# Kernel optimization log

Hardware: AMD Instinct MI355X
Metric: run time of the kernel (lower is better)

## Reference

```python
import jax, jax.numpy as jnp
import numpy as np

BN_EPS = 1e-5
B, N, C, H, HID = 16, 1024, 512, 8, 2048


def _bn(x, g, b, m, v):
    # inference-mode BatchNorm1d over channel dim (last axis here, since the
    # torch code transposes to (B,C,N) before BN and back after)
    return (x - m) * (g * jax.lax.rsqrt(v + BN_EPS)) + b


def _stage(x, w, bias, g, be, m, v):
    # Linear -> BN -> ReLU fused chain
    return jax.nn.relu(_bn(x @ w.T + bias, g, be, m, v))


def setup_inputs() -> dict:
    key = jax.random.key(0)
    ks = iter(jax.random.split(key, 64))
    d = {"x": jax.random.normal(next(ks), (B, N, C), dtype=jnp.float32)}

    def lin_bn(pref, out_f, in_f):
        d[pref + "_w"] = jax.random.normal(next(ks), (out_f, in_f), dtype=jnp.float32) * 0.02
        d[pref + "_b"] = jax.random.normal(next(ks), (out_f,), dtype=jnp.float32) * 0.02
        d[pref + "_g"] = 1.0 + 0.1 * jax.random.normal(next(ks), (out_f,), dtype=jnp.float32)
        d[pref + "_be"] = 0.1 * jax.random.normal(next(ks), (out_f,), dtype=jnp.float32)
        d[pref + "_m"] = 0.1 * jax.random.normal(next(ks), (out_f,), dtype=jnp.float32)
        d[pref + "_v"] = jax.random.uniform(next(ks), (out_f,), dtype=jnp.float32, minval=0.5, maxval=1.5)

    for p in ("q", "k", "v", "p"):
        lin_bn(p, C, C)
    lin_bn("f1", HID, C)
    lin_bn("f2", C, HID)
    return d


def reference(x, q_w, q_b, q_g, q_be, q_m, q_v,
              k_w, k_b, k_g, k_be, k_m, k_v,
              v_w, v_b, v_g, v_be, v_m, v_v,
              p_w, p_b, p_g, p_be, p_m, p_v,
              f1_w, f1_b, f1_g, f1_be, f1_m, f1_v,
              f2_w, f2_b, f2_g, f2_be, f2_m, f2_v):
    b, n, c = x.shape
    hd = c // H

    def heads(t):  # (B,N,C) -> (B,H,N,hd)
        return t.reshape(b, n, H, hd).transpose(0, 2, 1, 3)

    q = heads(_stage(x, q_w, q_b, q_g, q_be, q_m, q_v))
    k = heads(_stage(x, k_w, k_b, k_g, k_be, k_m, k_v))
    v = heads(_stage(x, v_w, v_b, v_g, v_be, v_m, v_v))

    # non-softmax linear attention: (q k^T * 0.125) v
    attn = jnp.einsum('bhqd,bhkd->bhqk', q, k) * 0.125
    o = jnp.einsum('bhqk,bhkd->bhqd', attn, v)
    o = o.transpose(0, 2, 1, 3).reshape(b, n, c)
    o = jax.nn.relu(o)  # attn_lif

    x1 = x + _stage(o, p_w, p_b, p_g, p_be, p_m, p_v)  # residual 1

    h = _stage(x1, f1_w, f1_b, f1_g, f1_be, f1_m, f1_v)
    y = _stage(h, f2_w, f2_b, f2_g, f2_be, f2_m, f2_v)
    return x1 + y  # residual 2
```

## Files before the change

kernel.cpp:

```cpp
#include <hip/hip_runtime.h>
#include <stdint.h>


typedef __attribute__((ext_vector_type(8))) short short8;
typedef __attribute__((ext_vector_type(4))) short short4v;
typedef __attribute__((ext_vector_type(4))) float f32x4;
typedef __attribute__((ext_vector_type(4))) unsigned int uint4v;

#define MFMA_BF16 __builtin_amdgcn_mfma_f32_16x16x32_bf16

__device__ __forceinline__ float bf2f(unsigned short u) {
    return __uint_as_float(((unsigned int)u) << 16);
}
__device__ __forceinline__ unsigned short f2bf(float f) {
    unsigned int b = __float_as_uint(f);
    return (unsigned short)((b + 0x7fffu + ((b >> 16) & 1u)) >> 16);
}
__device__ __forceinline__ void gl_lds16(const void* g, void* l) {
    __builtin_amdgcn_global_load_lds(
        (const __attribute__((address_space(1))) void*)g,
        (__attribute__((address_space(3))) void*)l, 16, 0, 0);
}

__global__ __launch_bounds__(256) void prep_bn(
    const float* __restrict__ bias, const float* __restrict__ g,
    const float* __restrict__ be,   const float* __restrict__ m,
    const float* __restrict__ v,
    float* __restrict__ sc, float* __restrict__ sh, int n)
{
    int i = blockIdx.x * 256 + threadIdx.x;
    if (i < n) {
        float s = g[i] * rsqrtf(v[i] + 1e-5f);
        sc[i] = s;
        sh[i] = (bias[i] - m[i]) * s + be[i];
    }
}

__global__ __launch_bounds__(256) void to_bf16(
    const float* __restrict__ in, unsigned short* __restrict__ out, int n8)
{
    int i = blockIdx.x * 256 + threadIdx.x;
    if (i >= n8) return;
    const float4* p = (const float4*)in + (size_t)i * 2;
    float4 a = p[0], b = p[1];
    short8 r = {(short)f2bf(a.x), (short)f2bf(a.y), (short)f2bf(a.z), (short)f2bf(a.w),
                (short)f2bf(b.x), (short)f2bf(b.y), (short)f2bf(b.z), (short)f2bf(b.w)};
    ((short8*)out)[i] = r;
}

__global__ __launch_bounds__(256) void prep_w(
    const float* __restrict__ W, unsigned short* __restrict__ ph, int N, int K)
{
    int tid = blockIdx.x * 256 + threadIdx.x;
    int KC = K >> 5;
    int total = (N >> 4) * KC * 64;
    if (tid >= total) return;
    int lane = tid & 63;
    int blk  = tid >> 6;
    int kc   = blk % KC;
    int n16  = blk / KC;
    int n  = (n16 << 4) + (lane & 15);
    int k0 = (kc << 5) + ((lane >> 4) << 3);
    const float* src = W + (size_t)n * K + k0;
    size_t dst = ((size_t)blk << 9) + (size_t)lane * 8;
#pragma unroll
    for (int j = 0; j < 8; ++j) ph[dst + j] = f2bf(src[j]);
}

template<int NT, int RESMODE, int OUTMODE>
__global__ __launch_bounds__(256) void gemm_bf16(
    const unsigned short* __restrict__ Ag, const unsigned short* __restrict__ Wg,
    const float* __restrict__ sc, const float* __restrict__ sh,
    const float* __restrict__ resf, const unsigned short* __restrict__ resb,
    float* __restrict__ outf, unsigned short* __restrict__ outb,
    unsigned short* __restrict__ oq, unsigned short* __restrict__ ok2,
    unsigned short* __restrict__ ov, int M, int N, int K)
{
    constexpr int NF = NT / 32;
    __shared__ unsigned short As[128 * 32];

    const int t    = threadIdx.x;
    const int lane = t & 63;
    const int w    = t >> 6;
    const int wm   = w >> 1, wn = w & 1;
    const int KC   = K >> 5;

    const int nx  = gridDim.x;
    const int nwg = nx * gridDim.y;
    int bid = blockIdx.y * nx + blockIdx.x;
    bid = (bid & 7) * (nwg >> 3) + (bid >> 3);
    const int m0 = (bid / nx) * 128;
    const int n0 = (bid % nx) * NT;

    const int sr  = lane >> 2;
    const int kbu = (lane & 3) ^ ((lane >> 3) & 3);
    const unsigned short* sA0 = Ag + (size_t)(m0 + w * 32 + sr) * K + kbu * 8;
    const unsigned short* sA1 = sA0 + (size_t)16 * K;
    unsigned short* dA0 = &As[(w * 32) * 32];
    unsigned short* dA1 = &As[(w * 32 + 16) * 32];

    const unsigned short* pB[NF];
#pragma unroll
    for (int nf = 0; nf < NF; ++nf) {
        const int n16 = (n0 >> 4) + wn * (NT / 32) + nf;
        pB[nf] = Wg + (((size_t)n16 * KC) << 9) + (size_t)lane * 8;
    }

    const int fr = lane & 15, fk = lane >> 4;
    const int funit = fk ^ ((fr >> 1) & 3);
    int aoff[4];
#pragma unroll
    for (int mi = 0; mi < 4; ++mi)
        aoff[mi] = (wm * 64 + mi * 16 + fr) * 32 + funit * 8;

    f32x4 acc[4][NF];
#pragma unroll
    for (int i = 0; i < 4; ++i)
#pragma unroll
        for (int j = 0; j < NF; ++j) acc[i][j] = f32x4{0.f, 0.f, 0.f, 0.f};

    for (int kc = 0; kc < KC; ++kc) {
        __syncthreads();
        gl_lds16(sA0, dA0); gl_lds16(sA1, dA1);
        sA0 += 32; sA1 += 32;

        short8 bh[NF];
#pragma unroll
        for (int nf = 0; nf < NF; ++nf) {
            bh[nf] = *(const short8*)pB[nf];
            pB[nf] += 512;
        }
        __syncthreads();

        short8 ah[4];
#pragma unroll
        for (int mi = 0; mi < 4; ++mi) ah[mi] = *(const short8*)&As[aoff[mi]];
#pragma unroll
        for (int mi = 0; mi < 4; ++mi)
#pragma unroll
            for (int nf = 0; nf < NF; ++nf)
                acc[mi][nf] = MFMA_BF16(ah[mi], bh[nf], acc[mi][nf], 0, 0, 0);
    }

    const int erow4 = fk * 4;
#pragma unroll
    for (int nf = 0; nf < NF; ++nf) {
        const int col = n0 + wn * (NT / 2) + nf * 16 + fr;
        const float scv = sc[col], shv = sh[col];
        unsigned short* qsplit = nullptr;
        int lc = 0;
        if (OUTMODE == 2) {
            const int tsel = col >> 9;
            qsplit = (tsel == 0) ? oq : (tsel == 1) ? ok2 : ov;
            lc = col & 511;
        }
#pragma unroll
        for (int mi = 0; mi < 4; ++mi) {
            const int rbase = m0 + wm * 64 + mi * 16 + erow4;
#pragma unroll
            for (int r = 0; r < 4; ++r) {
                const size_t row = (size_t)(rbase + r);
                float z = fmaf(acc[mi][nf][r], scv, shv);
                z = fmaxf(z, 0.f);
                if (RESMODE == 1) z += resf[row * N + col];
                if (RESMODE == 2) z += bf2f(resb[row * N + col]);
                if (OUTMODE == 0)      outb[row * N + col] = f2bf(z);
                else if (OUTMODE == 1) outf[row * N + col] = z;
                else                   qsplit[row * 512 + lc] = f2bf(z);
            }
        }
    }
}

__global__ __launch_bounds__(64) void attn_kv(
    const unsigned short* __restrict__ k, const unsigned short* __restrict__ v,
    unsigned short* __restrict__ ktvB)
{
    __shared__ unsigned short kN[32 * 66];
    __shared__ unsigned short vN[32 * 66];
    __shared__ float red[64 * 65];

    const int l  = threadIdx.x;
    const int bh = blockIdx.x >> 1;
    const int h1 = blockIdx.x & 1;
    const int b = bh >> 3, h = bh & 7;
    const int c8 = l & 7;
    const int rh = l >> 3;
    const int c  = l & 15, nh = l >> 4;

    f32x4 acc[4][4];
#pragma unroll
    for (int i = 0; i < 4; ++i)
#pragma unroll
        for (int j = 0; j < 4; ++j) acc[i][j] = f32x4{0.f, 0.f, 0.f, 0.f};

    const size_t gbase = ((size_t)b * 1024 + (size_t)h1 * 512) * 512 + (size_t)h * 64;

    for (int t = 0; t < 16; ++t) {
        short8 kr[4], vr[4];
#pragma unroll
        for (int q = 0; q < 4; ++q) {
            const int n = 8 * q + rh;
            const size_t ga = gbase + (size_t)(t * 32 + n) * 512 + c8 * 8;
            kr[q] = *(const short8*)(k + ga);
            vr[q] = *(const short8*)(v + ga);
        }
        __syncthreads();
#pragma unroll
        for (int q = 0; q < 4; ++q) {
            const int n = 8 * q + rh;
            unsigned int* pk = (unsigned int*)&kN[n * 66 + c8 * 8];
            unsigned int* pv = (unsigned int*)&vN[n * 66 + c8 * 8];
            uint4v ku = *(const uint4v*)&kr[q];
            uint4v vu = *(const uint4v*)&vr[q];
#pragma unroll
            for (int w2 = 0; w2 < 4; ++w2) { pk[w2] = ku[w2]; pv[w2] = vu[w2]; }
        }
        __syncthreads();

        short8 aF[4], bF[4];
#pragma unroll
        for (int it = 0; it < 4; ++it)
#pragma unroll
            for (int jj = 0; jj < 8; ++jj)
                aF[it][jj] = (short)kN[(8 * nh + jj) * 66 + it * 16 + c];
#pragma unroll
        for (int jt = 0; jt < 4; ++jt)
#pragma unroll
            for (int jj = 0; jj < 8; ++jj)
                bF[jt][jj] = (short)vN[(8 * nh + jj) * 66 + jt * 16 + c];
#pragma unroll
        for (int it = 0; it < 4; ++it)
#pragma unroll
            for (int jt = 0; jt < 4; ++jt)
                acc[it][jt] = MFMA_BF16(aF[it], bF[jt], acc[it][jt], 0, 0, 0);
    }

#pragma unroll
    for (int it = 0; it < 4; ++it)
#pragma unroll
        for (int jt = 0; jt < 4; ++jt)
#pragma unroll
            for (int r = 0; r < 4; ++r)
                red[(it * 16 + nh * 4 + r) * 65 + jt * 16 + c] = acc[it][jt][r];
    __syncthreads();

    unsigned short* dstb = ktvB + (size_t)bh * 8192;
#pragma unroll
    for (int j16 = 0; j16 < 4; ++j16)
#pragma unroll
        for (int dcl = 0; dcl < 2; ++dcl) {
            short8 o8;
#pragma unroll
            for (int jj = 0; jj < 8; ++jj)
                o8[jj] = (short)f2bf(red[(dcl * 32 + 8 * nh + jj) * 65 + j16 * 16 + c] * 0.125f);
            *(short8*)(dstb + (size_t)(j16 * 4 + (2 * h1 + dcl)) * 512 + l * 8) = o8;
        }
}

__global__ __launch_bounds__(256) void attn_qo(
    const unsigned short* __restrict__ q, const unsigned short* __restrict__ ktvB,
    unsigned short* __restrict__ o)
{
    __shared__ unsigned short qS[128 * 64];

    int bid = blockIdx.x;
    bid = (bid & 7) * 128 + (bid >> 3);
    const int bh = bid >> 3, mt = bid & 7;
    const int b = bh >> 3, h = bh & 7;
    const size_t Mbase = (size_t)b * 1024 + (size_t)mt * 128;
    const int t = threadIdx.x, l = t & 63, w = t >> 6;
    const int c = l & 15, nh = l >> 4;

#pragma unroll
    for (int qq = 0; qq < 4; ++qq) {
        const int r  = qq * 32 + w * 8 + (l >> 3);
        const int cl = (l & 7) ^ (r & 7);
        gl_lds16(q + (Mbase + r) * 512 + h * 64 + cl * 8,
                 &qS[(qq * 32 + w * 8) * 64]);
    }
    __syncthreads();

    const unsigned short* pB = ktvB + (size_t)bh * 8192 + (size_t)l * 8;

    f32x4 acc[2][4];
#pragma unroll
    for (int i = 0; i < 2; ++i)
#pragma unroll
        for (int j = 0; j < 4; ++j) acc[i][j] = f32x4{0.f, 0.f, 0.f, 0.f};

#pragma unroll
    for (int ks = 0; ks < 4; ++ks) {
        short8 aF[2], bF[4];
#pragma unroll
        for (int it = 0; it < 2; ++it) {
            const int ra   = w * 32 + it * 16 + c;
            const int phys = (((ks & 1) * 4) + nh) ^ (c & 7);
            aF[it] = *(const short8*)&qS[ra * 64 + phys * 8];
        }
#pragma unroll
        for (int jt = 0; jt < 4; ++jt)
            bF[jt] = *(const short8*)(pB + (size_t)(jt * 4 + ks) * 512);
#pragma unroll
        for (int it = 0; it < 2; ++it)
#pragma unroll
            for (int jt = 0; jt < 4; ++jt)
                acc[it][jt] = MFMA_BF16(aF[it], bF[jt], acc[it][jt], 0, 0, 0);
    }

#pragma unroll
    for (int it = 0; it < 2; ++it)
#pragma unroll
        for (int jt = 0; jt < 4; ++jt)
#pragma unroll
            for (int r = 0; r < 4; ++r) {
                const size_t row = Mbase + w * 32 + it * 16 + nh * 4 + r;
                o[row * 512 + h * 64 + jt * 16 + c] =
                    f2bf(fmaxf(acc[it][jt][r], 0.f));
            }
}

extern "C" void kernel_launch(void* const* d_in, const int* in_sizes, int n_in,
                              void* d_out, int out_size, void* d_ws, size_t ws_size,
                              hipStream_t stream)
{
    (void)in_sizes; (void)n_in; (void)out_size; (void)ws_size;
    const float* x = (const float*)d_in[0];
    auto P = [&](int i) { return (const float*)d_in[i]; };

    char* wsb = (char*)d_ws;
    const size_t MB = 1024 * 1024;
    auto US = [&](size_t off) { return (unsigned short*)(wsb + off); };

    unsigned short* Wqkv = US(0);
    unsigned short* Wp   = US(2 * MB);
    unsigned short* W1   = US(3 * MB);
    unsigned short* W2   = US(5 * MB);

    float* bn = (float*)(wsb + 7 * MB);
    float* sc_qkv = bn;          float* sh_qkv = bn + 1536;
    float* sc_p = bn + 3072;     float* sh_p = bn + 3584;
    float* sc_1 = bn + 4096;     float* sh_1 = bn + 6144;
    float* sc_2 = bn + 8192;     float* sh_2 = bn + 8704;

    unsigned short* xb = US(8 * MB);
    unsigned short* qb = US(25 * MB);
    unsigned short* kb = US(42 * MB);
    unsigned short* vb = US(59 * MB);
    unsigned short* hb = US(76 * MB);
    unsigned short* x1 = xb;
    unsigned short* ktvB = US(150 * MB);

    prep_bn<<<2, 256, 0, stream>>>(P(2),  P(3),  P(4),  P(5),  P(6),  sc_qkv,        sh_qkv,        512);
    prep_bn<<<2, 256, 0, stream>>>(P(8),  P(9),  P(10), P(11), P(12), sc_qkv + 512,  sh_qkv + 512,  512);
    prep_bn<<<2, 256, 0, stream>>>(P(14), P(15), P(16), P(17), P(18), sc_qkv + 1024, sh_qkv + 1024, 512);
    prep_bn<<<2, 256, 0, stream>>>(P(20), P(21), P(22), P(23), P(24), sc_p, sh_p, 512);
    prep_bn<<<8, 256, 0, stream>>>(P(26), P(27), P(28), P(29), P(30), sc_1, sh_1, 2048);
    prep_bn<<<2, 256, 0, stream>>>(P(32), P(33), P(34), P(35), P(36), sc_2, sh_2, 512);

    to_bf16<<<4096, 256, 0, stream>>>(x, xb, 16384 * 512 / 8);

    prep_w<<<128, 256, 0, stream>>>(P(1),  Wqkv,          512, 512);
    prep_w<<<128, 256, 0, stream>>>(P(7),  Wqkv + 262144, 512, 512);
    prep_w<<<128, 256, 0, stream>>>(P(13), Wqkv + 524288, 512, 512);
    prep_w<<<128, 256, 0, stream>>>(P(19), Wp, 512, 512);
    prep_w<<<512, 256, 0, stream>>>(P(25), W1, 2048, 512);
    prep_w<<<512, 256, 0, stream>>>(P(31), W2, 512, 2048);

    const dim3 blk(256);

    gemm_bf16<128, 0, 2><<<dim3(12, 128), blk, 0, stream>>>(
        xb, Wqkv, sc_qkv, sh_qkv, nullptr, nullptr,
        nullptr, nullptr, qb, kb, vb, 16384, 1536, 512);

    attn_kv<<<256, 64, 0, stream>>>(kb, vb, ktvB);
    attn_qo<<<1024, blk, 0, stream>>>(qb, ktvB, qb);

    gemm_bf16<64, 1, 0><<<dim3(8, 128), blk, 0, stream>>>(
        qb, Wp, sc_p, sh_p, x, nullptr,
        nullptr, x1, nullptr, nullptr, nullptr, 16384, 512, 512);

    gemm_bf16<128, 0, 0><<<dim3(16, 128), blk, 0, stream>>>(
        x1, W1, sc_1, sh_1, nullptr, nullptr,
        nullptr, hb, nullptr, nullptr, nullptr, 16384, 2048, 512);

    gemm_bf16<64, 2, 1><<<dim3(8, 128), blk, 0, stream>>>(
        hb, W2, sc_2, sh_2, nullptr, x1,
        (float*)d_out, nullptr, nullptr, nullptr, nullptr, 16384, 512, 2048);
}
```

Baseline: 375.9 us.

## Double-buffer A tile in LDS and prefetch B fragments in GEMM

The GEMM main loop now uses two LDS buffers for the A tile and register double-buffering for B fragments. The next k-chunk is issued before the MFMAs on the current one, and the loop drops to one barrier per iteration, so global-to-LDS latency can overlap with compute. Separately, the projection GEMM now reads its residual from the bf16 copy of x instead of fp32 x, which cuts residual read bandwidth but adds bf16 rounding to the residual path. The extra LDS buffer and the bnext registers raise resource use and could lower occupancy.

```diff
diff --git a/kernel.cpp b/kernel.cpp
--- a/kernel.cpp
+++ b/kernel.cpp
@@ -77,7 +77,7 @@
     unsigned short* __restrict__ ov, int M, int N, int K)
 {
     constexpr int NF = NT / 32;
-    __shared__ unsigned short As[128 * 32];
+    __shared__ unsigned short As[2][128 * 32];
 
     const int t    = threadIdx.x;
     const int lane = t & 63;
@@ -96,14 +96,14 @@
     const int kbu = (lane & 3) ^ ((lane >> 3) & 3);
     const unsigned short* sA0 = Ag + (size_t)(m0 + w * 32 + sr) * K + kbu * 8;
     const unsigned short* sA1 = sA0 + (size_t)16 * K;
-    unsigned short* dA0 = &As[(w * 32) * 32];
-    unsigned short* dA1 = &As[(w * 32 + 16) * 32];
+    const int dOf0 = (w * 32) * 32;
+    const int dOf1 = (w * 32 + 16) * 32;
 
     const unsigned short* pB[NF];
 #pragma unroll
     for (int nf = 0; nf < NF; ++nf) {
         const int n16 = (n0 >> 4) + wn * (NT / 32) + nf;
-        pB[nf] = Wg + (((size_t)n16 * KC) << 9) + (size_t)lane * 8;
+        pB[nf] = Wg + (((size_t)n16 * (K >> 5)) << 9) + (size_t)lane * 8;
     }
 
     const int fr = lane & 15, fk = lane >> 4;
@@ -119,27 +119,41 @@
 #pragma unroll
         for (int j = 0; j < NF; ++j) acc[i][j] = f32x4{0.f, 0.f, 0.f, 0.f};
 
+    gl_lds16(sA0, &As[0][dOf0]); gl_lds16(sA1, &As[0][dOf1]);
+    sA0 += 32; sA1 += 32;
+    short8 bcur[NF], bnext[NF];
+#pragma unroll
+    for (int nf = 0; nf < NF; ++nf) {
+        bcur[nf] = *(const short8*)pB[nf];
+        pB[nf] += 512;
+    }
+    __syncthreads();
+
+    int cur = 0;
     for (int kc = 0; kc < KC; ++kc) {
+        if (kc + 1 < KC) {
+            gl_lds16(sA0, &As[cur ^ 1][dOf0]);
+            gl_lds16(sA1, &As[cur ^ 1][dOf1]);
+            sA0 += 32; sA1 += 32;
+#pragma unroll
+            for (int nf = 0; nf < NF; ++nf) {
+                bnext[nf] = *(const short8*)pB[nf];
+                pB[nf] += 512;
+            }
+        }
+        short8 ah[4];
+#pragma unroll
+        for (int mi = 0; mi < 4; ++mi)
+            ah[mi] = *(const short8*)&As[cur][aoff[mi]];
+#pragma unroll
+        for (int mi = 0; mi < 4; ++mi)
+#pragma unroll
+            for (int nf = 0; nf < NF; ++nf)
+                acc[mi][nf] = MFMA_BF16(ah[mi], bcur[nf], acc[mi][nf], 0, 0, 0);
         __syncthreads();
-        gl_lds16(sA0, dA0); gl_lds16(sA1, dA1);
-        sA0 += 32; sA1 += 32;
-
-        short8 bh[NF];
-#pragma unroll
-        for (int nf = 0; nf < NF; ++nf) {
-            bh[nf] = *(const short8*)pB[nf];
-            pB[nf] += 512;
-        }
-        __syncthreads();
-
-        short8 ah[4];
-#pragma unroll
-        for (int mi = 0; mi < 4; ++mi) ah[mi] = *(const short8*)&As[aoff[mi]];
-#pragma unroll
-        for (int mi = 0; mi < 4; ++mi)
-#pragma unroll
-            for (int nf = 0; nf < NF; ++nf)
-                acc[mi][nf] = MFMA_BF16(ah[mi], bh[nf], acc[mi][nf], 0, 0, 0);
+#pragma unroll
+        for (int nf = 0; nf < NF; ++nf) bcur[nf] = bnext[nf];
+        cur ^= 1;
     }
 
     const int erow4 = fk * 4;
@@ -376,8 +390,8 @@
     attn_kv<<<256, 64, 0, stream>>>(kb, vb, ktvB);
     attn_qo<<<1024, blk, 0, stream>>>(qb, ktvB, qb);
 
-    gemm_bf16<64, 1, 0><<<dim3(8, 128), blk, 0, stream>>>(
-        qb, Wp, sc_p, sh_p, x, nullptr,
+    gemm_bf16<64, 2, 0><<<dim3(8, 128), blk, 0, stream>>>(
+        qb, Wp, sc_p, sh_p, nullptr, xb,
         nullptr, x1, nullptr, nullptr, nullptr, 16384, 512, 512);
 
     gemm_bf16<128, 0, 0><<<dim3(16, 128), blk, 0, stream>>>(
```

Result: slower. 389.1 us (+3.5%).
